# Performance work log

Hardware: AMD Instinct MI355X
Metric: run time of the kernel (lower is better)

The kernel has to match this reference:

```python
import jax, jax.numpy as jnp
import numpy as np

N_NODES = 50000
N_EDGES = 800000
IN_DIM, HID, OUT_DIM = 32, 96, 1
NEG_SLOPE = 0.2


def _glorot(key, shape):
    fan_in, fan_out = shape[0], shape[-1]
    lim = float(np.sqrt(6.0 / (fan_in + fan_out)))
    return jax.random.uniform(key, shape, jnp.float32, -lim, lim)


def setup_inputs() -> dict:
    key = jax.random.key(0)
    ks = jax.random.split(key, 20)
    inp = {
        "x": jax.random.normal(ks[0], (N_NODES, IN_DIM), jnp.float32),
        "edge_index": jax.random.randint(ks[1], (2, N_EDGES), 0, N_NODES, jnp.int64),
        "edge_weight": jax.random.uniform(ks[2], (N_EDGES,), jnp.float32),
    }
    dims = [(IN_DIM, HID), (HID, HID), (HID, HID), (HID, OUT_DIM)]
    names = ["0", "1", "2", "f"]
    k = 3
    for nm, (di, do) in zip(names, dims):
        inp["W" + nm] = _glorot(ks[k], (di, do)); k += 1
        inp["as" + nm] = _glorot(ks[k], (1, do))[0]; k += 1
        inp["ad" + nm] = _glorot(ks[k], (1, do))[0]; k += 1
        inp["b" + nm] = jnp.zeros((do,), jnp.float32)
    return inp


def _gat_conv(x, src, dst, n, W, a_s, a_d, b):
    # h: [N, out]; per-node attention logits, gathered per edge
    h = x @ W
    es = h @ a_s  # [N]
    ed = h @ a_d  # [N]
    e = jax.nn.leaky_relu(es[src] + ed[dst], NEG_SLOPE)  # [E]
    m = jax.ops.segment_max(e, dst, num_segments=n)  # segment-softmax (stable)
    ex = jnp.exp(e - m[dst])
    s = jax.ops.segment_sum(ex, dst, num_segments=n)
    alpha = ex / s[dst]  # every node has a self loop -> s > 0
    out = jax.ops.segment_sum(alpha[:, None] * h[src], dst, num_segments=n)
    return out + b


def reference(x, edge_index, edge_weight, W0, as0, ad0, b0, W1, as1, ad1, b1,
              W2, as2, ad2, b2, Wf, asf, adf, bf):
    # edge_weight is ignored: PyG GATConv with edge_dim=None drops edge_attr.
    n = x.shape[0]
    loops = jnp.arange(n, dtype=edge_index.dtype)
    src = jnp.concatenate([edge_index[0], loops])  # add_self_loops=True
    dst = jnp.concatenate([edge_index[1], loops])

    # dropout is identity in eval mode
    for (W, a_s, a_d, b) in [(W0, as0, ad0, b0), (W1, as1, ad1, b1), (W2, as2, ad2, b2)]:
        residual = x
        x = _gat_conv(x, src, dst, n, W, a_s, a_d, b)
        if x.shape == residual.shape:
            x = x + residual
        x = jax.nn.relu(x)
    return _gat_conv(x, src, dst, n, Wf, asf, adf, bf)
```

## Files before the change

### kernel.cpp

```cpp
#include <hip/hip_runtime.h>
#include <hip/hip_fp16.h>
#include <math.h>

#define N_NODES 50000
#define N_EDGES 800000
#define E_TOT   (N_EDGES + N_NODES)
#define IN_DIM  32
#define HID     96
#define NEG_SLOPE 0.2f
#define BUCKET  48
#define G_PAD   50
#define NBINS   196
#define BCAP    5120
#define GC_STRIDE 64
#define FILL_EPT 4
#define FILL_NB ((N_EDGES + 256 * FILL_EPT - 1) / (256 * FILL_EPT))
#define AGG_BLOCKS (N_NODES / 16)
#define PREP_BLOCKS ((N_NODES * 32) / 256)
#define WT_BLOCKS (((HID * HID) + 255) / 256)

typedef _Float16 half8v __attribute__((ext_vector_type(8)));
typedef float    float4v __attribute__((ext_vector_type(4)));

static inline int cdiv(long long a, int b) { return (int)((a + b - 1) / b); }

__device__ __forceinline__ int clamp_src(int s) {
    return (int)min((unsigned)s, (unsigned)(N_NODES - 1));
}

__global__ __launch_bounds__(256) void build_prep_kernel(
    const int* __restrict__ ei, unsigned* __restrict__ gcnt,
    unsigned* __restrict__ ebuf,
    const float* __restrict__ x, const float* __restrict__ W0,
    const float* __restrict__ as0, const float* __restrict__ ad0,
    __half* __restrict__ xh, float* __restrict__ es, float* __restrict__ ed,
    const float* __restrict__ W1, const float* __restrict__ W2,
    __half* __restrict__ WT1, __half* __restrict__ WT2) {
    int b = blockIdx.x;
    if (b < FILL_NB) {
        __shared__ unsigned lcnt[256];
        __shared__ unsigned lbase[256];
        int tid = threadIdx.x;
        lcnt[tid] = 0u;
        __syncthreads();
        int e0 = (b * 256 + tid) * FILL_EPT;
        bool val = e0 < N_EDGES;
        int binv[FILL_EPT]; unsigned rank[FILL_EPT], pk[FILL_EPT];
        if (val) {
            int4 d4 = *(const int4*)(ei + N_EDGES + e0);
            int4 s4 = *(const int4*)(ei + e0);
            int dd[4] = {d4.x, d4.y, d4.z, d4.w};
            int ss[4] = {s4.x, s4.y, s4.z, s4.w};
            #pragma unroll
            for (int k = 0; k < FILL_EPT; ++k) {
                int d = clamp_src(dd[k]);
                binv[k] = d >> 8;
                pk[k] = (unsigned)clamp_src(ss[k]) | ((unsigned)(d & 255) << 16);
                rank[k] = atomicAdd(&lcnt[binv[k]], 1u);
            }
        }
        __syncthreads();
        if (tid < NBINS) {
            unsigned c = lcnt[tid];
            lbase[tid] = c ? atomicAdd(gcnt + (size_t)tid * GC_STRIDE, c) : 0u;
        }
        __syncthreads();
        if (val) {
            #pragma unroll
            for (int k = 0; k < FILL_EPT; ++k) {
                unsigned pos = lbase[binv[k]] + rank[k];
                if (pos < BCAP) ebuf[(size_t)binv[k] * BCAP + pos] = pk[k];
            }
        }
        return;
    }
    b -= FILL_NB;
    if (b >= PREP_BLOCKS) {
        int i = (b - PREP_BLOCKS) * 256 + threadIdx.x;
        if (i < HID * HID) {
            int n = i / HID, k = i - n * HID;
            WT1[i] = __float2half(W1[k * HID + n]);
            WT2[i] = __float2half(W2[k * HID + n]);
        }
        return;
    }
    __shared__ float s_us[32], s_ud[32];
    if (threadIdx.x < 64) {
        int k = threadIdx.x & 31;
        int sel = threadIdx.x >> 5;
        const float* a = sel ? ad0 : as0;
        float acc = 0.f;
        #pragma unroll 8
        for (int c = 0; c < HID; ++c) acc += W0[k * HID + c] * a[c];
        if (sel) s_ud[k] = acc; else s_us[k] = acc;
    }
    __syncthreads();
    int idx = b * 256 + threadIdx.x;
    int node = idx >> 5;
    int k = threadIdx.x & 31;
    float xv = x[(size_t)node * 32 + k];
    float xnb = __shfl_xor(xv, 1);
    if ((k & 1) == 0) {
        __half2 h2v = __floats2half2_rn(xv, xnb);
        ((__half2*)xh)[((size_t)node * 32 + k) >> 1] = h2v;
    }
    float ps = xv * s_us[k], pd = xv * s_ud[k];
    #pragma unroll
    for (int o = 16; o; o >>= 1) {
        ps += __shfl_xor(ps, o);
        pd += __shfl_xor(pd, o);
    }
    if (k == 0) { es[node] = ps; ed[node] = pd; }
}

__global__ __launch_bounds__(256) void bucket_build_kernel(
    const unsigned* __restrict__ gcnt, const unsigned* __restrict__ ebuf,
    unsigned* __restrict__ cnt, unsigned short* __restrict__ srcs) {
    __shared__ unsigned short lsr[256][BUCKET];
    __shared__ unsigned lct[256];
    int bin = blockIdx.x, tid = threadIdx.x;
    int nb = bin * 256 + tid;
    lct[tid] = 1u;
    lsr[tid][0] = (unsigned short)min(nb, N_NODES - 1);
    __syncthreads();
    unsigned ec = min(gcnt[(size_t)bin * GC_STRIDE], (unsigned)BCAP);
    for (unsigned j = tid; j < ec; j += 256) {
        unsigned pkv = ebuf[(size_t)bin * BCAP + j];
        unsigned dloc = (pkv >> 16) & 255u;
        unsigned pos = atomicAdd(&lct[dloc], 1u);
        if (pos < BUCKET) lsr[dloc][pos] = (unsigned short)(pkv & 0xFFFFu);
    }
    __syncthreads();
    if (nb < N_NODES) cnt[nb] = min(lct[tid], (unsigned)BUCKET);
    const uint4* ls4 = (const uint4*)&lsr[0][0];
    uint4* gs4 = (uint4*)(srcs + (size_t)bin * 256 * BUCKET);
    for (int i = tid; i < 256 * (BUCKET / 8); i += 256) {
        int node = i / (BUCKET / 8);
        if (bin * 256 + node < N_NODES) gs4[i] = ls4[i];
    }
}

__global__ __launch_bounds__(256) void aggregate32_kernel(
    const unsigned* __restrict__ cnt, const unsigned short* __restrict__ srcs,
    const float* __restrict__ es, const float* __restrict__ ed,
    const __half* __restrict__ xh, float* __restrict__ agg) {
    __shared__ uint2 sh[4][4][G_PAD];
    int lane = threadIdx.x & 63;
    int wv = threadIdx.x >> 6;
    int g = lane >> 4, lin = lane & 15;
    int node = blockIdx.x * 16 + wv * 4 + g;
    size_t row = (size_t)node * BUCKET;
    int deg = min((int)cnt[node], BUCKET);
    float edv = ed[node];

    float lsum = 0.f;
    float4 acc = {0.f, 0.f, 0.f, 0.f};
    const uint2* x2 = (const uint2*)xh;
    int h8sel = lin >> 3;
    int c = lin & 7;

    for (int j = lin; j < deg; j += 16) {
        int s = clamp_src(srcs[row + j]);
        float v = es[s] + edv;
        v = v > 0.f ? v : NEG_SLOPE * v;
        float e = __expf(v);
        uint2 p; p.x = (unsigned)s; p.y = __float_as_uint(e);
        sh[wv][g][j] = p;
        lsum += e;
    }
    int j = 0;
    for (; j + 4 <= deg; j += 4) {
        uint2 p0 = sh[wv][g][j + h8sel];
        uint2 p1 = sh[wv][g][j + 2 + h8sel];
        uint2 q0 = x2[(size_t)p0.x * 8 + c];
        uint2 q1 = x2[(size_t)p1.x * 8 + c];
        float e0 = __uint_as_float(p0.y), e1 = __uint_as_float(p1.y);
        float2 f00 = __half22float2(*(__half2*)&q0.x);
        float2 f01 = __half22float2(*(__half2*)&q0.y);
        float2 f10 = __half22float2(*(__half2*)&q1.x);
        float2 f11 = __half22float2(*(__half2*)&q1.y);
        acc.x += e0 * f00.x + e1 * f10.x; acc.y += e0 * f00.y + e1 * f10.y;
        acc.z += e0 * f01.x + e1 * f11.x; acc.w += e0 * f01.y + e1 * f11.y;
    }
    for (; j < deg; j += 2) {
        int idx = j + h8sel;
        if (idx < deg) {
            uint2 p = sh[wv][g][idx];
            uint2 q = x2[(size_t)p.x * 8 + c];
            float e = __uint_as_float(p.y);
            float2 f0 = __half22float2(*(__half2*)&q.x);
            float2 f1 = __half22float2(*(__half2*)&q.y);
            acc.x += e * f0.x; acc.y += e * f0.y;
            acc.z += e * f1.x; acc.w += e * f1.y;
        }
    }
    #pragma unroll
    for (int o = 1; o < 16; o <<= 1) lsum += __shfl_xor(lsum, o);
    acc.x += __shfl_xor(acc.x, 8);
    acc.y += __shfl_xor(acc.y, 8);
    acc.z += __shfl_xor(acc.z, 8);
    acc.w += __shfl_xor(acc.w, 8);
    if (lin < 8) {
        float inv = 1.f / lsum;
        float4 o4; o4.x = acc.x * inv; o4.y = acc.y * inv; o4.z = acc.z * inv; o4.w = acc.w * inv;
        ((float4*)agg)[(size_t)node * 8 + lin] = o4;
    }
}

__global__ void gemm32_kernel(const float* __restrict__ agg, const float* __restrict__ W,
                              const float* __restrict__ b, __half* __restrict__ out16) {
    int idx = blockIdx.x * blockDim.x + threadIdx.x;
    if (idx >= (N_NODES / 4) * 24) return;
    int g   = idx / 24;
    int c4q = idx - g * 24;
    int n0 = g * 4;
    const float4* Xa = (const float4*)agg + (size_t)n0 * 8;
    const float4* Xb = Xa + 8;
    const float4* Xc = Xb + 8;
    const float4* Xd = Xc + 8;
    const float4* W4 = (const float4*)W;

    float4 accA = {0,0,0,0}, accB = {0,0,0,0}, accC = {0,0,0,0}, accD = {0,0,0,0};
    for (int k4 = 0; k4 < 8; ++k4) {
        float4 xa = Xa[k4], xb = Xb[k4], xc = Xc[k4], xd = Xd[k4];
        #pragma unroll
        for (int kk = 0; kk < 4; ++kk) {
            float4 w = W4[(size_t)(k4 * 4 + kk) * 24 + c4q];
            float sa = ((const float*)&xa)[kk], sb = ((const float*)&xb)[kk];
            float sc = ((const float*)&xc)[kk], sd = ((const float*)&xd)[kk];
            accA.x += sa * w.x; accA.y += sa * w.y; accA.z += sa * w.z; accA.w += sa * w.w;
            accB.x += sb * w.x; accB.y += sb * w.y; accB.z += sb * w.z; accB.w += sb * w.w;
            accC.x += sc * w.x; accC.y += sc * w.y; accC.z += sc * w.z; accC.w += sc * w.w;
            accD.x += sd * w.x; accD.y += sd * w.y; accD.z += sd * w.z; accD.w += sd * w.w;
        }
    }
    float4 bb = ((const float4*)b)[c4q];
    uint2* O16 = (uint2*)out16;
    #pragma unroll
    for (int nn = 0; nn < 4; ++nn) {
        float4 a = (nn == 0) ? accA : (nn == 1) ? accB : (nn == 2) ? accC : accD;
        float rx = fmaxf(a.x + bb.x, 0.f), ry = fmaxf(a.y + bb.y, 0.f);
        float rz = fmaxf(a.z + bb.z, 0.f), rw = fmaxf(a.w + bb.w, 0.f);
        __half2 q0 = __floats2half2_rn(rx, ry), q1 = __floats2half2_rn(rz, rw);
        uint2 st; st.x = *(unsigned*)&q0; st.y = *(unsigned*)&q1;
        O16[(size_t)(n0 + nn) * 24 + c4q] = st;
    }
}

__global__ __launch_bounds__(256) void mfma_gemm96_kernel(
    const __half* __restrict__ x16, const __half* __restrict__ wt,
    const float* __restrict__ a_s, const float* __restrict__ a_d,
    __half* __restrict__ h, float* __restrict__ es, float* __restrict__ ed) {
    __shared__ __align__(16) __half s_t[4][16][104];
    int wid = (int)((blockIdx.x * 256 + threadIdx.x) >> 6);
    if (wid >= N_NODES / 16) return;
    int lane = threadIdx.x & 63;
    int wvl = threadIdx.x >> 6;
    int col = lane & 15, quad = lane >> 4;
    int m0 = wid * 16;
    const __half* arow = x16 + (size_t)(m0 + col) * 96 + quad * 8;
    const __half* brow = wt + (size_t)col * 96 + quad * 8;

    float4v acc[6];
    #pragma unroll
    for (int t = 0; t < 6; ++t) acc[t] = (float4v){0.f, 0.f, 0.f, 0.f};

    #pragma unroll
    for (int ks = 0; ks < 3; ++ks) {
        half8v afrag = *(const half8v*)(arow + ks * 32);
        #pragma unroll
        for (int t = 0; t < 6; ++t) {
            half8v bfrag = *(const half8v*)(brow + (size_t)t * 16 * 96 + ks * 32);
            acc[t] = __builtin_amdgcn_mfma_f32_16x16x32_f16(afrag, bfrag, acc[t], 0, 0, 0);
        }
    }

    float ps0 = 0.f, ps1 = 0.f, ps2 = 0.f, ps3 = 0.f;
    float pd0 = 0.f, pd1 = 0.f, pd2 = 0.f, pd3 = 0.f;
    #pragma unroll
    for (int t = 0; t < 6; ++t) {
        int ch = t * 16 + col;
        float sa = a_s[ch], sd = a_d[ch];
        float v0 = acc[t][0], v1 = acc[t][1], v2 = acc[t][2], v3 = acc[t][3];
        int r0 = quad * 4;
        s_t[wvl][r0 + 0][ch] = __float2half(v0);
        s_t[wvl][r0 + 1][ch] = __float2half(v1);
        s_t[wvl][r0 + 2][ch] = __float2half(v2);
        s_t[wvl][r0 + 3][ch] = __float2half(v3);
        ps0 += v0 * sa; ps1 += v1 * sa; ps2 += v2 * sa; ps3 += v3 * sa;
        pd0 += v0 * sd; pd1 += v1 * sd; pd2 += v2 * sd; pd3 += v3 * sd;
    }
    #pragma unroll
    for (int o = 1; o < 16; o <<= 1) {
        ps0 += __shfl_xor(ps0, o); ps1 += __shfl_xor(ps1, o);
        ps2 += __shfl_xor(ps2, o); ps3 += __shfl_xor(ps3, o);
        pd0 += __shfl_xor(pd0, o); pd1 += __shfl_xor(pd1, o);
        pd2 += __shfl_xor(pd2, o); pd3 += __shfl_xor(pd3, o);
    }
    if (col == 0) {
        int nb = m0 + quad * 4;
        es[nb] = ps0; es[nb + 1] = ps1; es[nb + 2] = ps2; es[nb + 3] = ps3;
        ed[nb] = pd0; ed[nb + 1] = pd1; ed[nb + 2] = pd2; ed[nb + 3] = pd3;
    }
    {
        int trow = lane >> 2, q = lane & 3;
        const uint4* sr = (const uint4*)&s_t[wvl][trow][0];
        uint4* H8 = (uint4*)h;
        size_t rb = (size_t)(m0 + trow) * 12;
        H8[rb + q]     = sr[q];
        H8[rb + q + 4] = sr[q + 4];
        H8[rb + q + 8] = sr[q + 8];
    }
}

__global__ __launch_bounds__(256) void aggregate96_kernel(
    const unsigned* __restrict__ cnt, const unsigned short* __restrict__ srcs,
    const float* __restrict__ es, const float* __restrict__ ed,
    const __half* __restrict__ h, const float* __restrict__ b,
    const __half* __restrict__ res16, __half* __restrict__ out16,
    const float* __restrict__ Wf, float* __restrict__ hfin, int do_relu) {
    __shared__ uint2 sh[4][4][G_PAD];
    int lane = threadIdx.x & 63;
    int wv = threadIdx.x >> 6;
    int g = lane >> 4, lin = lane & 15;
    int node = blockIdx.x * 16 + wv * 4 + g;
    size_t row = (size_t)node * BUCKET;
    int deg = min((int)cnt[node], BUCKET);
    float edv = ed[node];

    float lsum = 0.f;
    float a0 = 0.f, a1 = 0.f, a2 = 0.f, a3 = 0.f, a4 = 0.f, a5 = 0.f, a6 = 0.f, a7 = 0.f;
    const uint4* h8 = (const uint4*)h;
    bool act = (lin < 12);

    for (int j = lin; j < deg; j += 16) {
        int s = clamp_src(srcs[row + j]);
        float v = es[s] + edv;
        v = v > 0.f ? v : NEG_SLOPE * v;
        float e = __expf(v);
        uint2 p; p.x = (unsigned)s; p.y = __float_as_uint(e);
        sh[wv][g][j] = p;
        lsum += e;
    }
    int j = 0;
    for (; j + 2 <= deg; j += 2) {
        uint2 p0 = sh[wv][g][j];
        uint2 p1 = sh[wv][g][j + 1];
        if (act) {
            uint4 q0 = h8[(size_t)p0.x * 12 + lin];
            uint4 q1 = h8[(size_t)p1.x * 12 + lin];
            float e0 = __uint_as_float(p0.y), e1 = __uint_as_float(p1.y);
            float2 fa0 = __half22float2(*(__half2*)&q0.x);
            float2 fa1 = __half22float2(*(__half2*)&q0.y);
            float2 fa2 = __half22float2(*(__half2*)&q0.z);
            float2 fa3 = __half22float2(*(__half2*)&q0.w);
            float2 fb0 = __half22float2(*(__half2*)&q1.x);
            float2 fb1 = __half22float2(*(__half2*)&q1.y);
            float2 fb2 = __half22float2(*(__half2*)&q1.z);
            float2 fb3 = __half22float2(*(__half2*)&q1.w);
            a0 += e0 * fa0.x + e1 * fb0.x; a1 += e0 * fa0.y + e1 * fb0.y;
            a2 += e0 * fa1.x + e1 * fb1.x; a3 += e0 * fa1.y + e1 * fb1.y;
            a4 += e0 * fa2.x + e1 * fb2.x; a5 += e0 * fa2.y + e1 * fb2.y;
            a6 += e0 * fa3.x + e1 * fb3.x; a7 += e0 * fa3.y + e1 * fb3.y;
        }
    }
    if (j < deg) {
        uint2 p = sh[wv][g][j];
        if (act) {
            uint4 q = h8[(size_t)p.x * 12 + lin];
            float e = __uint_as_float(p.y);
            float2 f0 = __half22float2(*(__half2*)&q.x);
            float2 f1 = __half22float2(*(__half2*)&q.y);
            float2 f2 = __half22float2(*(__half2*)&q.z);
            float2 f3 = __half22float2(*(__half2*)&q.w);
            a0 += e * f0.x; a1 += e * f0.y;
            a2 += e * f1.x; a3 += e * f1.y;
            a4 += e * f2.x; a5 += e * f2.y;
            a6 += e * f3.x; a7 += e * f3.y;
        }
    }
    #pragma unroll
    for (int o = 1; o < 16; o <<= 1) lsum += __shfl_xor(lsum, o);

    float pfin = 0.f;
    if (act) {
        float inv = 1.f / lsum;
        const float4* b4 = (const float4*)b;
        float4 bb0 = b4[lin * 2], bb1 = b4[lin * 2 + 1];
        float v0 = a0 * inv + bb0.x, v1 = a1 * inv + bb0.y;
        float v2 = a2 * inv + bb0.z, v3 = a3 * inv + bb0.w;
        float v4 = a4 * inv + bb1.x, v5 = a5 * inv + bb1.y;
        float v6 = a6 * inv + bb1.z, v7 = a7 * inv + bb1.w;
        if (res16) {
            uint4 rr = ((const uint4*)res16)[(size_t)node * 12 + lin];
            float2 r0 = __half22float2(*(__half2*)&rr.x);
            float2 r1 = __half22float2(*(__half2*)&rr.y);
            float2 r2 = __half22float2(*(__half2*)&rr.z);
            float2 r3 = __half22float2(*(__half2*)&rr.w);
            v0 += r0.x; v1 += r0.y; v2 += r1.x; v3 += r1.y;
            v4 += r2.x; v5 += r2.y; v6 += r3.x; v7 += r3.y;
        }
        if (do_relu) {
            v0 = fmaxf(v0, 0.f); v1 = fmaxf(v1, 0.f); v2 = fmaxf(v2, 0.f); v3 = fmaxf(v3, 0.f);
            v4 = fmaxf(v4, 0.f); v5 = fmaxf(v5, 0.f); v6 = fmaxf(v6, 0.f); v7 = fmaxf(v7, 0.f);
        }
        if (out16) {
            __half2 q0 = __floats2half2_rn(v0, v1), q1 = __floats2half2_rn(v2, v3);
            __half2 q2 = __floats2half2_rn(v4, v5), q3 = __floats2half2_rn(v6, v7);
            uint4 st; st.x = *(unsigned*)&q0; st.y = *(unsigned*)&q1;
            st.z = *(unsigned*)&q2; st.w = *(unsigned*)&q3;
            ((uint4*)out16)[(size_t)node * 12 + lin] = st;
        }
        if (hfin) {
            const float4* w4 = (const float4*)Wf;
            float4 wf0 = w4[lin * 2], wf1 = w4[lin * 2 + 1];
            pfin = v0 * wf0.x + v1 * wf0.y + v2 * wf0.z + v3 * wf0.w
                 + v4 * wf1.x + v5 * wf1.y + v6 * wf1.z + v7 * wf1.w;
        }
    }
    if (hfin) {
        #pragma unroll
        for (int o = 1; o < 16; o <<= 1) pfin += __shfl_xor(pfin, o);
        if (lin == 0) hfin[node] = pfin;
    }
}

__global__ __launch_bounds__(256) void aggregate1_kernel(
    const unsigned* __restrict__ cnt, const unsigned short* __restrict__ srcs,
    const float* __restrict__ hfin, const float* __restrict__ asf,
    const float* __restrict__ adf, const float* __restrict__ bf,
    float* __restrict__ out) {
    int lane = threadIdx.x & 63;
    int wv = threadIdx.x >> 6;
    int g = lane >> 4, lin = lane & 15;
    int node = blockIdx.x * 16 + wv * 4 + g;
    size_t row = (size_t)node * BUCKET;
    int deg = min((int)cnt[node], BUCKET);
    float as0 = asf[0], ad0 = adf[0];
    float edv = hfin[node] * ad0;

    float lsum = 0.f, acc = 0.f;
    for (int j = lin; j < deg; j += 16) {
        int s = clamp_src(srcs[row + j]);
        float hs = hfin[s];
        float v = as0 * hs + edv;
        v = v > 0.f ? v : NEG_SLOPE * v;
        float ex = __expf(v);
        lsum += ex;
        acc += ex * hs;
    }
    #pragma unroll
    for (int o = 1; o < 16; o <<= 1) {
        lsum += __shfl_xor(lsum, o);
        acc  += __shfl_xor(acc, o);
    }
    if (lin == 0) out[node] = acc / lsum + bf[0];
}


extern "C" void kernel_launch(void* const* d_in, const int* in_sizes, int n_in,
                              void* d_out, int out_size, void* d_ws, size_t ws_size,
                              hipStream_t stream) {
    const float* x  = (const float*)d_in[0];
    const int*   ei = (const int*)d_in[1];
    const float* W0 = (const float*)d_in[3];
    const float* as0 = (const float*)d_in[4];
    const float* ad0 = (const float*)d_in[5];
    const float* b0 = (const float*)d_in[6];
    const float* W1 = (const float*)d_in[7];
    const float* as1 = (const float*)d_in[8];
    const float* ad1 = (const float*)d_in[9];
    const float* b1 = (const float*)d_in[10];
    const float* W2 = (const float*)d_in[11];
    const float* as2 = (const float*)d_in[12];
    const float* ad2 = (const float*)d_in[13];
    const float* b2 = (const float*)d_in[14];
    const float* Wf = (const float*)d_in[15];
    const float* asf = (const float*)d_in[16];
    const float* adf = (const float*)d_in[17];
    const float* bf = (const float*)d_in[18];

    float* out = (float*)d_out;

    float* Hf = (float*)d_ws;
    __half* H16 = (__half*)Hf;
    float* ES = Hf + (long long)N_NODES * HID;
    float* ED = ES + N_NODES;
    unsigned* CNT = (unsigned*)(ED + N_NODES);
    unsigned short* SRCS = (unsigned short*)(CNT + N_NODES);
    __half* X16A = (__half*)(SRCS + (size_t)N_NODES * BUCKET);
    __half* X16B = X16A + (size_t)N_NODES * HID;
    __half* WT1 = X16B + (size_t)N_NODES * HID;
    __half* WT2 = WT1 + HID * HID;
    float* HFIN = (float*)(WT2 + HID * HID);
    __half* XH = (__half*)(HFIN + N_NODES);
    unsigned* GCNT = (unsigned*)(XH + (size_t)N_NODES * 32);
    unsigned* EBUF = GCNT + (size_t)NBINS * GC_STRIDE;
    float* AGG = (float*)Hf;

    hipMemsetAsync(GCNT, 0, (size_t)NBINS * GC_STRIDE * sizeof(unsigned), stream);
    build_prep_kernel<<<FILL_NB + PREP_BLOCKS + WT_BLOCKS, 256, 0, stream>>>(
        ei, GCNT, EBUF, x, W0, as0, ad0, XH, ES, ED, W1, W2, WT1, WT2);
    bucket_build_kernel<<<NBINS, 256, 0, stream>>>(GCNT, EBUF, CNT, SRCS);

    const int gemm_threads = (N_NODES / 4) * 24;
    const int mfma_blocks = cdiv(N_NODES / 16, 4);

    aggregate32_kernel<<<AGG_BLOCKS, 256, 0, stream>>>(CNT, SRCS, ES, ED, XH, AGG);
    gemm32_kernel<<<cdiv(gemm_threads, 256), 256, 0, stream>>>(AGG, W0, b0, X16A);

    mfma_gemm96_kernel<<<mfma_blocks, 256, 0, stream>>>(X16A, WT1, as1, ad1, H16, ES, ED);
    aggregate96_kernel<<<AGG_BLOCKS, 256, 0, stream>>>(
        CNT, SRCS, ES, ED, H16, b1, X16A, X16B, nullptr, nullptr, 1);

    mfma_gemm96_kernel<<<mfma_blocks, 256, 0, stream>>>(X16B, WT2, as2, ad2, H16, ES, ED);
    aggregate96_kernel<<<AGG_BLOCKS, 256, 0, stream>>>(
        CNT, SRCS, ES, ED, H16, b2, X16B, nullptr, Wf, HFIN, 1);

    aggregate1_kernel<<<AGG_BLOCKS, 256, 0, stream>>>(CNT, SRCS, HFIN, asf, adf, bf, out);
}
```

Before: 259.0 us.

## Fuse layer-0 GEMM into aggregation, widen edge fill, unroll gather loops

Folds the 32->96 layer-0 projection, bias and ReLU into aggregate32_kernel. Each block stages W0 and its 16 aggregated rows in shared memory, so the float AGG buffer round trip and a separate launch are gone. The edge-binning fill now handles 16 edges per thread with the bin packed into the key, and the gather loops in both aggregate kernels are unrolled deeper to keep more loads in flight. The costs are more shared memory and register pressure per block, which can lower occupancy, plus a reload of W0 into every block.

```diff
diff --git a/kernel.cpp b/kernel.cpp
--- a/kernel.cpp
+++ b/kernel.cpp
@@ -13,7 +13,7 @@
 #define NBINS   196
 #define BCAP    5120
 #define GC_STRIDE 64
-#define FILL_EPT 4
+#define FILL_EPT 16
 #define FILL_NB ((N_EDGES + 256 * FILL_EPT - 1) / (256 * FILL_EPT))
 #define AGG_BLOCKS (N_NODES / 16)
 #define PREP_BLOCKS ((N_NODES * 32) / 256)
@@ -45,18 +45,23 @@
         __syncthreads();
         int e0 = (b * 256 + tid) * FILL_EPT;
         bool val = e0 < N_EDGES;
-        int binv[FILL_EPT]; unsigned rank[FILL_EPT], pk[FILL_EPT];
+        unsigned pk[FILL_EPT];
+        unsigned short rank[FILL_EPT];
         if (val) {
-            int4 d4 = *(const int4*)(ei + N_EDGES + e0);
-            int4 s4 = *(const int4*)(ei + e0);
-            int dd[4] = {d4.x, d4.y, d4.z, d4.w};
-            int ss[4] = {s4.x, s4.y, s4.z, s4.w};
             #pragma unroll
-            for (int k = 0; k < FILL_EPT; ++k) {
-                int d = clamp_src(dd[k]);
-                binv[k] = d >> 8;
-                pk[k] = (unsigned)clamp_src(ss[k]) | ((unsigned)(d & 255) << 16);
-                rank[k] = atomicAdd(&lcnt[binv[k]], 1u);
+            for (int q = 0; q < FILL_EPT / 4; ++q) {
+                int4 d4 = *(const int4*)(ei + N_EDGES + e0 + q * 4);
+                int4 s4 = *(const int4*)(ei + e0 + q * 4);
+                int dd[4] = {d4.x, d4.y, d4.z, d4.w};
+                int ss[4] = {s4.x, s4.y, s4.z, s4.w};
+                #pragma unroll
+                for (int k = 0; k < 4; ++k) {
+                    int d = clamp_src(dd[k]);
+                    int bin = d >> 8;
+                    pk[q * 4 + k] = (unsigned)clamp_src(ss[k]) | ((unsigned)(d & 255) << 16)
+                                  | ((unsigned)bin << 24);
+                    rank[q * 4 + k] = (unsigned short)atomicAdd(&lcnt[bin], 1u);
+                }
             }
         }
         __syncthreads();
@@ -68,8 +73,9 @@
         if (val) {
             #pragma unroll
             for (int k = 0; k < FILL_EPT; ++k) {
-                unsigned pos = lbase[binv[k]] + rank[k];
-                if (pos < BCAP) ebuf[(size_t)binv[k] * BCAP + pos] = pk[k];
+                unsigned bin = pk[k] >> 24;
+                unsigned pos = lbase[bin] + rank[k];
+                if (pos < BCAP) ebuf[(size_t)bin * BCAP + pos] = pk[k];
             }
         }
         return;
@@ -143,8 +149,16 @@
 __global__ __launch_bounds__(256) void aggregate32_kernel(
     const unsigned* __restrict__ cnt, const unsigned short* __restrict__ srcs,
     const float* __restrict__ es, const float* __restrict__ ed,
-    const __half* __restrict__ xh, float* __restrict__ agg) {
+    const __half* __restrict__ xh,
+    const float* __restrict__ W0, const float* __restrict__ b0,
+    __half* __restrict__ x16a) {
     __shared__ uint2 sh[4][4][G_PAD];
+    __shared__ float s_ag[16][33];
+    __shared__ float4 s_w0[32][24];
+    const float4* W4g = (const float4*)W0;
+    for (int i = threadIdx.x; i < 32 * 24; i += 256)
+        s_w0[i / 24][i % 24] = W4g[i];
+
     int lane = threadIdx.x & 63;
     int wv = threadIdx.x >> 6;
     int g = lane >> 4, lin = lane & 15;
@@ -169,16 +183,34 @@
         lsum += e;
     }
     int j = 0;
+    for (; j + 8 <= deg; j += 8) {
+        uint2 p0 = sh[wv][g][j + h8sel];
+        uint2 p1 = sh[wv][g][j + 2 + h8sel];
+        uint2 p2 = sh[wv][g][j + 4 + h8sel];
+        uint2 p3 = sh[wv][g][j + 6 + h8sel];
+        uint2 q0 = x2[(size_t)p0.x * 8 + c];
+        uint2 q1 = x2[(size_t)p1.x * 8 + c];
+        uint2 q2 = x2[(size_t)p2.x * 8 + c];
+        uint2 q3 = x2[(size_t)p3.x * 8 + c];
+        float e0 = __uint_as_float(p0.y), e1 = __uint_as_float(p1.y);
+        float e2 = __uint_as_float(p2.y), e3 = __uint_as_float(p3.y);
+        float2 f00 = __half22float2(*(__half2*)&q0.x), f01 = __half22float2(*(__half2*)&q0.y);
+        float2 f10 = __half22float2(*(__half2*)&q1.x), f11 = __half22float2(*(__half2*)&q1.y);
+        float2 f20 = __half22float2(*(__half2*)&q2.x), f21 = __half22float2(*(__half2*)&q2.y);
+        float2 f30 = __half22float2(*(__half2*)&q3.x), f31 = __half22float2(*(__half2*)&q3.y);
+        acc.x += e0 * f00.x + e1 * f10.x + e2 * f20.x + e3 * f30.x;
+        acc.y += e0 * f00.y + e1 * f10.y + e2 * f20.y + e3 * f30.y;
+        acc.z += e0 * f01.x + e1 * f11.x + e2 * f21.x + e3 * f31.x;
+        acc.w += e0 * f01.y + e1 * f11.y + e2 * f21.y + e3 * f31.y;
+    }
     for (; j + 4 <= deg; j += 4) {
         uint2 p0 = sh[wv][g][j + h8sel];
         uint2 p1 = sh[wv][g][j + 2 + h8sel];
         uint2 q0 = x2[(size_t)p0.x * 8 + c];
         uint2 q1 = x2[(size_t)p1.x * 8 + c];
         float e0 = __uint_as_float(p0.y), e1 = __uint_as_float(p1.y);
-        float2 f00 = __half22float2(*(__half2*)&q0.x);
-        float2 f01 = __half22float2(*(__half2*)&q0.y);
-        float2 f10 = __half22float2(*(__half2*)&q1.x);
-        float2 f11 = __half22float2(*(__half2*)&q1.y);
+        float2 f00 = __half22float2(*(__half2*)&q0.x), f01 = __half22float2(*(__half2*)&q0.y);
+        float2 f10 = __half22float2(*(__half2*)&q1.x), f11 = __half22float2(*(__half2*)&q1.y);
         acc.x += e0 * f00.x + e1 * f10.x; acc.y += e0 * f00.y + e1 * f10.y;
         acc.z += e0 * f01.x + e1 * f11.x; acc.w += e0 * f01.y + e1 * f11.y;
     }
@@ -202,48 +234,35 @@
     acc.w += __shfl_xor(acc.w, 8);
     if (lin < 8) {
         float inv = 1.f / lsum;
-        float4 o4; o4.x = acc.x * inv; o4.y = acc.y * inv; o4.z = acc.z * inv; o4.w = acc.w * inv;
-        ((float4*)agg)[(size_t)node * 8 + lin] = o4;
-    }
-}
-
-__global__ void gemm32_kernel(const float* __restrict__ agg, const float* __restrict__ W,
-                              const float* __restrict__ b, __half* __restrict__ out16) {
-    int idx = blockIdx.x * blockDim.x + threadIdx.x;
-    if (idx >= (N_NODES / 4) * 24) return;
-    int g   = idx / 24;
-    int c4q = idx - g * 24;
-    int n0 = g * 4;
-    const float4* Xa = (const float4*)agg + (size_t)n0 * 8;
-    const float4* Xb = Xa + 8;
-    const float4* Xc = Xb + 8;
-    const float4* Xd = Xc + 8;
-    const float4* W4 = (const float4*)W;
-
-    float4 accA = {0,0,0,0}, accB = {0,0,0,0}, accC = {0,0,0,0}, accD = {0,0,0,0};
-    for (int k4 = 0; k4 < 8; ++k4) {
-        float4 xa = Xa[k4], xb = Xb[k4], xc = Xc[k4], xd = Xd[k4];
-        #pragma unroll
-        for (int kk = 0; kk < 4; ++kk) {
-            float4 w = W4[(size_t)(k4 * 4 + kk) * 24 + c4q];
-            float sa = ((const float*)&xa)[kk], sb = ((const float*)&xb)[kk];
-            float sc = ((const float*)&xc)[kk], sd = ((const float*)&xd)[kk];
-            accA.x += sa * w.x; accA.y += sa * w.y; accA.z += sa * w.z; accA.w += sa * w.w;
-            accB.x += sb * w.x; accB.y += sb * w.y; accB.z += sb * w.z; accB.w += sb * w.w;
-            accC.x += sc * w.x; accC.y += sc * w.y; accC.z += sc * w.z; accC.w += sc * w.w;
-            accD.x += sd * w.x; accD.y += sd * w.y; accD.z += sd * w.z; accD.w += sd * w.w;
-        }
-    }
-    float4 bb = ((const float4*)b)[c4q];
-    uint2* O16 = (uint2*)out16;
-    #pragma unroll
-    for (int nn = 0; nn < 4; ++nn) {
-        float4 a = (nn == 0) ? accA : (nn == 1) ? accB : (nn == 2) ? accC : accD;
-        float rx = fmaxf(a.x + bb.x, 0.f), ry = fmaxf(a.y + bb.y, 0.f);
-        float rz = fmaxf(a.z + bb.z, 0.f), rw = fmaxf(a.w + bb.w, 0.f);
-        __half2 q0 = __floats2half2_rn(rx, ry), q1 = __floats2half2_rn(rz, rw);
-        uint2 st; st.x = *(unsigned*)&q0; st.y = *(unsigned*)&q1;
-        O16[(size_t)(n0 + nn) * 24 + c4q] = st;
+        int n = wv * 4 + g;
+        s_ag[n][lin * 4 + 0] = acc.x * inv;
+        s_ag[n][lin * 4 + 1] = acc.y * inv;
+        s_ag[n][lin * 4 + 2] = acc.z * inv;
+        s_ag[n][lin * 4 + 3] = acc.w * inv;
+    }
+    __syncthreads();
+    int t = threadIdx.x;
+    if (t < 192) {
+        int n = t / 12, c8 = t - n * 12;
+        int onode = blockIdx.x * 16 + n;
+        float4 a0v = {0.f, 0.f, 0.f, 0.f}, a1v = {0.f, 0.f, 0.f, 0.f};
+        #pragma unroll 8
+        for (int k = 0; k < 32; ++k) {
+            float a = s_ag[n][k];
+            float4 w0 = s_w0[k][c8 * 2], w1 = s_w0[k][c8 * 2 + 1];
+            a0v.x += a * w0.x; a0v.y += a * w0.y; a0v.z += a * w0.z; a0v.w += a * w0.w;
+            a1v.x += a * w1.x; a1v.y += a * w1.y; a1v.z += a * w1.z; a1v.w += a * w1.w;
+        }
+        float4 bb0 = ((const float4*)b0)[c8 * 2], bb1 = ((const float4*)b0)[c8 * 2 + 1];
+        float v0 = fmaxf(a0v.x + bb0.x, 0.f), v1 = fmaxf(a0v.y + bb0.y, 0.f);
+        float v2 = fmaxf(a0v.z + bb0.z, 0.f), v3 = fmaxf(a0v.w + bb0.w, 0.f);
+        float v4 = fmaxf(a1v.x + bb1.x, 0.f), v5 = fmaxf(a1v.y + bb1.y, 0.f);
+        float v6 = fmaxf(a1v.z + bb1.z, 0.f), v7 = fmaxf(a1v.w + bb1.w, 0.f);
+        __half2 q0 = __floats2half2_rn(v0, v1), q1 = __floats2half2_rn(v2, v3);
+        __half2 q2 = __floats2half2_rn(v4, v5), q3 = __floats2half2_rn(v6, v7);
+        uint4 st; st.x = *(unsigned*)&q0; st.y = *(unsigned*)&q1;
+        st.z = *(unsigned*)&q2; st.w = *(unsigned*)&q3;
+        ((uint4*)x16a)[(size_t)onode * 12 + c8] = st;
     }
 }
 
@@ -343,28 +362,37 @@
         lsum += e;
     }
     int j = 0;
-    for (; j + 2 <= deg; j += 2) {
+    for (; j + 4 <= deg; j += 4) {
         uint2 p0 = sh[wv][g][j];
         uint2 p1 = sh[wv][g][j + 1];
+        uint2 p2 = sh[wv][g][j + 2];
+        uint2 p3 = sh[wv][g][j + 3];
         if (act) {
             uint4 q0 = h8[(size_t)p0.x * 12 + lin];
             uint4 q1 = h8[(size_t)p1.x * 12 + lin];
+            uint4 q2 = h8[(size_t)p2.x * 12 + lin];
+            uint4 q3 = h8[(size_t)p3.x * 12 + lin];
             float e0 = __uint_as_float(p0.y), e1 = __uint_as_float(p1.y);
-            float2 fa0 = __half22float2(*(__half2*)&q0.x);
-            float2 fa1 = __half22float2(*(__half2*)&q0.y);
-            float2 fa2 = __half22float2(*(__half2*)&q0.z);
-            float2 fa3 = __half22float2(*(__half2*)&q0.w);
-            float2 fb0 = __half22float2(*(__half2*)&q1.x);
-            float2 fb1 = __half22float2(*(__half2*)&q1.y);
-            float2 fb2 = __half22float2(*(__half2*)&q1.z);
-            float2 fb3 = __half22float2(*(__half2*)&q1.w);
-            a0 += e0 * fa0.x + e1 * fb0.x; a1 += e0 * fa0.y + e1 * fb0.y;
-            a2 += e0 * fa1.x + e1 * fb1.x; a3 += e0 * fa1.y + e1 * fb1.y;
-            a4 += e0 * fa2.x + e1 * fb2.x; a5 += e0 * fa2.y + e1 * fb2.y;
-            a6 += e0 * fa3.x + e1 * fb3.x; a7 += e0 * fa3.y + e1 * fb3.y;
-        }
-    }
-    if (j < deg) {
+            float e2 = __uint_as_float(p2.y), e3 = __uint_as_float(p3.y);
+            float2 fa0 = __half22float2(*(__half2*)&q0.x), fa1 = __half22float2(*(__half2*)&q0.y);
+            float2 fa2 = __half22float2(*(__half2*)&q0.z), fa3 = __half22float2(*(__half2*)&q0.w);
+            float2 fb0 = __half22float2(*(__half2*)&q1.x), fb1 = __half22float2(*(__half2*)&q1.y);
+            float2 fb2 = __half22float2(*(__half2*)&q1.z), fb3 = __half22float2(*(__half2*)&q1.w);
+            float2 fc0 = __half22float2(*(__half2*)&q2.x), fc1 = __half22float2(*(__half2*)&q2.y);
+            float2 fc2 = __half22float2(*(__half2*)&q2.z), fc3 = __half22float2(*(__half2*)&q2.w);
+            float2 fd0 = __half22float2(*(__half2*)&q3.x), fd1 = __half22float2(*(__half2*)&q3.y);
+            float2 fd2 = __half22float2(*(__half2*)&q3.z), fd3 = __half22float2(*(__half2*)&q3.w);
+            a0 += e0 * fa0.x + e1 * fb0.x + e2 * fc0.x + e3 * fd0.x;
+            a1 += e0 * fa0.y + e1 * fb0.y + e2 * fc0.y + e3 * fd0.y;
+            a2 += e0 * fa1.x + e1 * fb1.x + e2 * fc1.x + e3 * fd1.x;
+            a3 += e0 * fa1.y + e1 * fb1.y + e2 * fc1.y + e3 * fd1.y;
+            a4 += e0 * fa2.x + e1 * fb2.x + e2 * fc2.x + e3 * fd2.x;
+            a5 += e0 * fa2.y + e1 * fb2.y + e2 * fc2.y + e3 * fd2.y;
+            a6 += e0 * fa3.x + e1 * fb3.x + e2 * fc3.x + e3 * fd3.x;
+            a7 += e0 * fa3.y + e1 * fb3.y + e2 * fc3.y + e3 * fd3.y;
+        }
+    }
+    for (; j < deg; ++j) {
         uint2 p = sh[wv][g][j];
         if (act) {
             uint4 q = h8[(size_t)p.x * 12 + lin];
@@ -496,18 +524,15 @@
     __half* XH = (__half*)(HFIN + N_NODES);
     unsigned* GCNT = (unsigned*)(XH + (size_t)N_NODES * 32);
     unsigned* EBUF = GCNT + (size_t)NBINS * GC_STRIDE;
-    float* AGG = (float*)Hf;
 
     hipMemsetAsync(GCNT, 0, (size_t)NBINS * GC_STRIDE * sizeof(unsigned), stream);
     build_prep_kernel<<<FILL_NB + PREP_BLOCKS + WT_BLOCKS, 256, 0, stream>>>(
         ei, GCNT, EBUF, x, W0, as0, ad0, XH, ES, ED, W1, W2, WT1, WT2);
     bucket_build_kernel<<<NBINS, 256, 0, stream>>>(GCNT, EBUF, CNT, SRCS);
 
-    const int gemm_threads = (N_NODES / 4) * 24;
     const int mfma_blocks = cdiv(N_NODES / 16, 4);
 
-    aggregate32_kernel<<<AGG_BLOCKS, 256, 0, stream>>>(CNT, SRCS, ES, ED, XH, AGG);
-    gemm32_kernel<<<cdiv(gemm_threads, 256), 256, 0, stream>>>(AGG, W0, b0, X16A);
+    aggregate32_kernel<<<AGG_BLOCKS, 256, 0, stream>>>(CNT, SRCS, ES, ED, XH, W0, b0, X16A);
 
     mfma_gemm96_kernel<<<mfma_blocks, 256, 0, stream>>>(X16A, WT1, as1, ad1, H16, ES, ED);
     aggregate96_kernel<<<AGG_BLOCKS, 256, 0, stream>>>(
```

After: 239.2 us. -7.6%, faster.
